# Kernel optimization log

Measured on AMD Instinct MI355X. Metric: run time of the kernel, lower is better.

The kernel has to match this reference:

```python
import jax, jax.numpy as jnp
import numpy as np

N_NODES = 50000
N_EDGES = 800000
IN_FEATURES = 256
HIDDEN = 128


def setup_inputs() -> dict:
    key = jax.random.key(0)
    k_x, k_r, k_c, k_v, k_w, k_b = jax.random.split(key, 6)
    x = jax.random.normal(k_x, (N_NODES, IN_FEATURES), dtype=jnp.float32)
    adj_row = jax.random.randint(k_r, (N_EDGES,), 0, N_NODES, dtype=jnp.int32)
    adj_col = jax.random.randint(k_c, (N_EDGES,), 0, N_NODES, dtype=jnp.int32)
    adj_val = jax.random.uniform(k_v, (N_EDGES,), dtype=jnp.float32)
    # Linear params: weight [hidden, in_features] (xavier-normal-ish), bias [hidden]
    std = float(np.sqrt(2.0 / (IN_FEATURES + HIDDEN)))
    W = jax.random.normal(k_w, (HIDDEN, IN_FEATURES), dtype=jnp.float32) * std
    b = jax.random.normal(k_b, (HIDDEN,), dtype=jnp.float32) * 0.01
    return {"x": x, "adj_row": adj_row, "adj_col": adj_col, "adj_val": adj_val, "W": W, "b": b}


def reference(x, adj_row, adj_col, adj_val, W, b):
    # support = Linear(x): [N, hidden]
    support = jnp.einsum('nf,hf->nh', x, W) + b
    # sparse adj @ support via edge-list gather + segment-sum scatter
    gathered = support[adj_col] * adj_val[:, None]          # [E, hidden]
    out = jax.ops.segment_sum(gathered, adj_row, num_segments=N_NODES)  # [N, hidden]
    return out
```

## Files before the change

kernel.cpp:

```cpp
#include <hip/hip_runtime.h>

#define N_NODES 50000
#define N_EDGES 800000
#define IN_F    256
#define HIDDEN  128

#define BUCKET_SZ 128
#define NB        391
#define NBS       512
#define EBLOCK    2048
#define EBLOCKS   391
#define LBLOCKS   782
#define CAP       2500
#define OV_CAP    4096

typedef __attribute__((ext_vector_type(8))) short bf16x8;
typedef __attribute__((ext_vector_type(4))) float f32x4;

__device__ inline unsigned short f2bf(float f) {
    unsigned u = __float_as_uint(f);
    u += 0x7FFF + ((u >> 16) & 1);
    return (unsigned short)(u >> 16);
}
__device__ inline bf16x8 cvt8(float4 a, float4 b) {
    bf16x8 r;
    r[0] = (short)f2bf(a.x); r[1] = (short)f2bf(a.y);
    r[2] = (short)f2bf(a.z); r[3] = (short)f2bf(a.w);
    r[4] = (short)f2bf(b.x); r[5] = (short)f2bf(b.y);
    r[6] = (short)f2bf(b.z); r[7] = (short)f2bf(b.w);
    return r;
}
__device__ inline float bfLo(unsigned u) { return __uint_as_float(u << 16); }
__device__ inline float bfHi(unsigned u) { return __uint_as_float(u & 0xFFFF0000u); }

__global__ __launch_bounds__(256) void fused_linear_partition_kernel(
    const float* __restrict__ x, const float* __restrict__ W,
    const float* __restrict__ bias, unsigned short* __restrict__ support,
    const int* __restrict__ adj_row, const int* __restrict__ adj_col,
    const float* __restrict__ adj_val, int* __restrict__ cursor,
    int2* __restrict__ part, int4* __restrict__ ovbuf, int* __restrict__ ovcnt)
{
    __shared__ __align__(16) char smem[32768];
    const int tid = threadIdx.x;

    if (blockIdx.x < EBLOCKS) {
        int2* lbuf  = (int2*)smem;
        int*  lofs  = (int*)(smem + 16384);
        int*  lcur  = (int*)(smem + 18432);
        int*  gbase = (int*)(smem + 20480);
        int*  tsum  = (int*)(smem + 22528);

        const int base = blockIdx.x * EBLOCK;
        const int n    = min(EBLOCK, N_EDGES - base);

        for (int i = tid; i < NBS; i += 256) lofs[i] = 0;
        __syncthreads();

        unsigned pk[8]; float pv[8];
#pragma unroll
        for (int i = 0; i < 8; ++i) {
            int e = base + tid + i * 256;
            bool ok = e < N_EDGES;
            int ee = ok ? e : 0;
            int r = adj_row[ee], c = adj_col[ee];
            float v = adj_val[ee];
            if (ok) {
                unsigned bk = (unsigned)r >> 7;
                pk[i] = (bk << 23) | (((unsigned)r & 127u) << 16) | (unsigned)c;
                pv[i] = v;
                atomicAdd(&lofs[bk], 1);
            } else pk[i] = 0xFFFFFFFFu;
        }
        __syncthreads();

        int s0 = lofs[tid * 2], s1 = lofs[tid * 2 + 1];
        int mysum = s0 + s1;
        tsum[tid] = mysum;
        __syncthreads();
#pragma unroll
        for (int off = 1; off < 256; off <<= 1) {
            int t = (tid >= off) ? tsum[tid - off] : 0;
            __syncthreads();
            tsum[tid] += t;
            __syncthreads();
        }
        int ex = tsum[tid] - mysum;
        lofs[tid * 2]     = ex;
        lofs[tid * 2 + 1] = ex + s0;
        __syncthreads();

        for (int b = tid; b < NB; b += 256) {
            int nb2 = (b * 2 + 2 < NBS) ? lofs[b + 1] : n;
            int c = lofs[b + 1] - lofs[b];
            (void)nb2;
            gbase[b] = (c > 0) ? atomicAdd(&cursor[b], c) : 0;
            lcur[b]  = lofs[b];
        }
        __syncthreads();

#pragma unroll
        for (int i = 0; i < 8; ++i) {
            if (pk[i] != 0xFFFFFFFFu) {
                unsigned bk = pk[i] >> 23;
                int p = atomicAdd(&lcur[bk], 1);
                lbuf[p] = make_int2((int)pk[i], __float_as_int(pv[i]));
            }
        }
        __syncthreads();

        for (int j = tid; j < n; j += 256) {
            int2 cv = lbuf[j];
            unsigned bk = ((unsigned)cv.x) >> 23;
            int loc = gbase[bk] + (j - lofs[bk]);
            if (loc < CAP) {
                part[(size_t)bk * CAP + loc] = make_int2(cv.x & 0x7FFFFF, cv.y);
            } else {
                int op = atomicAdd(ovcnt, 1);
                if (op < OV_CAP) {
                    int r = (int)(bk * BUCKET_SZ) + ((cv.x >> 16) & 127);
                    ovbuf[op] = make_int4(r, cv.x & 0xFFFF, cv.y, 0);
                }
            }
        }
    } else {
        short* wfrag = (short*)smem;

        const int bid  = blockIdx.x - EBLOCKS;
        const int lane = tid & 63;
        const int wave = tid >> 6;
        const int quad = lane >> 4;
        const int l16  = lane & 15;

        int m = bid * 64 + wave * 16 + l16;
        if (m >= N_NODES) m = N_NODES - 1;
        const float* xrow = x + (size_t)m * IN_F;

        f32x4 acc[8];
#pragma unroll
        for (int s = 0; s < 8; ++s) acc[s] = (f32x4){0.f, 0.f, 0.f, 0.f};

#pragma unroll
        for (int half = 0; half < 2; ++half) {
#pragma unroll
            for (int it = 0; it < 8; ++it) {
                const int f   = it * 256 + tid;
                const int ln  = f & 63;
                const int s   = (f >> 6) & 7;
                const int kc  = f >> 9;
                const int row = s * 16 + (ln & 15);
                const int k0  = (half * 4 + kc) * 32 + (ln >> 4) * 8;
                const float* wp = W + (size_t)row * IN_F + k0;
                float4 b0 = *(const float4*)wp;
                float4 b1 = *(const float4*)(wp + 4);
                *(bf16x8*)(&wfrag[(size_t)f * 8]) = cvt8(b0, b1);
            }
            __syncthreads();

#pragma unroll
            for (int kc = 0; kc < 4; ++kc) {
                const int k0 = (half * 4 + kc) * 32 + quad * 8;
                float4 a0 = *(const float4*)(xrow + k0);
                float4 a1 = *(const float4*)(xrow + k0 + 4);
                bf16x8 af = cvt8(a0, a1);
                const short* bbase = &wfrag[((size_t)(kc * 8) * 64 + lane) * 8];
#pragma unroll
                for (int s = 0; s < 8; ++s) {
                    bf16x8 bf = *(const bf16x8*)(bbase + (size_t)s * 64 * 8);
                    acc[s] = __builtin_amdgcn_mfma_f32_16x16x32_bf16(af, bf, acc[s], 0, 0, 0);
                }
            }
            __syncthreads();
        }

        const int rowBase = bid * 64 + wave * 16 + quad * 4;
#pragma unroll
        for (int reg = 0; reg < 4; ++reg) {
            const int r = rowBase + reg;
            if (r < N_NODES) {
#pragma unroll
                for (int s = 0; s < 8; ++s) {
                    const int col = s * 16 + l16;
                    float v = acc[s][reg] + bias[col];
                    support[(size_t)r * HIDDEN + col] = f2bf(v);
                }
            }
        }
    }
}

__global__ __launch_bounds__(512) void bucket_gather_kernel(
    const int* __restrict__ cursor, const int2* __restrict__ part,
    const unsigned int* __restrict__ support_u32, float* __restrict__ out)
{
    __shared__ int2 sbuf[CAP];
    __shared__ int  hist[BUCKET_SZ];
    __shared__ int  rp[BUCKET_SZ + 1];
    __shared__ int  cur[BUCKET_SZ];

    const int tid  = threadIdx.x;
    const int b    = blockIdx.x;
    const int n    = min(cursor[b], CAP);
    const int wave = tid >> 6;
    const int lane = tid & 63;

    if (tid < BUCKET_SZ) hist[tid] = 0;
    __syncthreads();

    int2 held[(CAP + 511) / 512];
    int  nheld = 0;
    const int2* pb = part + (size_t)b * CAP;
    for (int j = tid; j < n; j += 512) {
        int2 cv = pb[j];
        held[nheld++] = cv;
        atomicAdd(&hist[(cv.x >> 16) & 127], 1);
    }
    __syncthreads();

    if (tid < 64) {
        int a = hist[tid], c = hist[tid + 64];
        int ia = a, ic = c;
#pragma unroll
        for (int off = 1; off < 64; off <<= 1) {
            int ta = __shfl_up(ia, off);
            int tc = __shfl_up(ic, off);
            if (tid >= off) { ia += ta; ic += tc; }
        }
        int totA = __shfl(ia, 63);
        rp[tid + 1]      = ia;
        rp[tid + 65]     = totA + ic;
        if (tid == 0) rp[0] = 0;
        cur[tid]      = ia - a;
        cur[tid + 64] = totA + ic - c;
    }
    __syncthreads();

    for (int i = 0; i < nheld; ++i) {
        int r = (held[i].x >> 16) & 127;
        int p = atomicAdd(&cur[r], 1);
        sbuf[p] = held[i];
    }
    __syncthreads();

    const int rowLo = wave * 16;
#pragma unroll 1
    for (int r = rowLo; r < rowLo + 16; ++r) {
        const int grow = b * BUCKET_SZ + r;
        if (grow >= N_NODES) break;
        const int s = rp[r], e = rp[r + 1];
        float ax = 0.f, ay = 0.f;
        int j = s;
        for (; j + 3 < e; j += 4) {
            int2 c0 = sbuf[j],     c1 = sbuf[j + 1];
            int2 c2 = sbuf[j + 2], c3 = sbuf[j + 3];
            unsigned u0 = support_u32[(size_t)(c0.x & 0xFFFF) * 64 + lane];
            unsigned u1 = support_u32[(size_t)(c1.x & 0xFFFF) * 64 + lane];
            unsigned u2 = support_u32[(size_t)(c2.x & 0xFFFF) * 64 + lane];
            unsigned u3 = support_u32[(size_t)(c3.x & 0xFFFF) * 64 + lane];
            float v0 = __int_as_float(c0.y), v1 = __int_as_float(c1.y);
            float v2 = __int_as_float(c2.y), v3 = __int_as_float(c3.y);
            ax += v0 * bfLo(u0); ay += v0 * bfHi(u0);
            ax += v1 * bfLo(u1); ay += v1 * bfHi(u1);
            ax += v2 * bfLo(u2); ay += v2 * bfHi(u2);
            ax += v3 * bfLo(u3); ay += v3 * bfHi(u3);
        }
        for (; j < e; ++j) {
            int2 cv = sbuf[j];
            unsigned u = support_u32[(size_t)(cv.x & 0xFFFF) * 64 + lane];
            float v = __int_as_float(cv.y);
            ax += v * bfLo(u); ay += v * bfHi(u);
        }
        *(float2*)(out + (size_t)grow * HIDDEN + lane * 2) = make_float2(ax, ay);
    }
}

__global__ __launch_bounds__(256) void overflow_fix_kernel(
    const int* __restrict__ ovcnt, const int4* __restrict__ ovbuf,
    const unsigned int* __restrict__ support_u32, float* __restrict__ out)
{
    const int n    = min(*ovcnt, OV_CAP);
    const int wave = threadIdx.x >> 6;
    const int lane = threadIdx.x & 63;
    for (int j = wave; j < n; j += 4) {
        int4 o = ovbuf[j];
        unsigned u = support_u32[(size_t)o.y * 64 + lane];
        float v = __int_as_float(o.z);
        unsafeAtomicAdd(out + (size_t)o.x * HIDDEN + lane * 2,     v * bfLo(u));
        unsafeAtomicAdd(out + (size_t)o.x * HIDDEN + lane * 2 + 1, v * bfHi(u));
    }
}

extern "C" void kernel_launch(void* const* d_in, const int* in_sizes, int n_in,
                              void* d_out, int out_size, void* d_ws, size_t ws_size,
                              hipStream_t stream) {
    const float* x       = (const float*)d_in[0];
    const int*   adj_row = (const int*)d_in[1];
    const int*   adj_col = (const int*)d_in[2];
    const float* adj_val = (const float*)d_in[3];
    const float* W       = (const float*)d_in[4];
    const float* b       = (const float*)d_in[5];
    float* out = (float*)d_out;

    char* wsb = (char*)d_ws;
    const size_t off_support = 0;
    const size_t off_part    = off_support + (size_t)N_NODES * HIDDEN * 2;
    const size_t off_cursor  = off_part + (size_t)NB * CAP * 8;
    const size_t off_ovcnt   = off_cursor + (size_t)NB * 4;
    const size_t off_ovbuf   = (off_ovcnt + 4 + 15) & ~(size_t)15;

    unsigned short* support = (unsigned short*)(wsb + off_support);
    int2* part   = (int2*)(wsb + off_part);
    int*  cursor = (int*)(wsb + off_cursor);
    int*  ovcnt  = (int*)(wsb + off_ovcnt);
    int4* ovbuf  = (int4*)(wsb + off_ovbuf);

    hipMemsetAsync(cursor, 0, (size_t)(NB + 1) * 4, stream);

    fused_linear_partition_kernel<<<EBLOCKS + LBLOCKS, 256, 0, stream>>>(
        x, W, b, support, adj_row, adj_col, adj_val, cursor, part, ovbuf, ovcnt);
    bucket_gather_kernel<<<NB, 512, 0, stream>>>(
        cursor, part, (const unsigned int*)support, out);
    overflow_fix_kernel<<<1, 256, 0, stream>>>(
        ovcnt, ovbuf, (const unsigned int*)support, out);
}
```

Before: 188.9 us.

## Halve bucket size to 64 rows and fold overflow handling into gather

Rows are now partitioned into 782 buckets of 64 rows instead of 391 of 128, with the bucket id packed into the top 10 bits. The partition scan widens to 1024 bins, with four bins per thread. The gather kernel gets twice as many blocks, so more CUs are kept busy on the latency-bound support gathers. It now reads its partition twice instead of holding entries in registers, and scans the overflow buffer inline per row. That replaces the separate atomic overflow kernel and saves one launch. The cost is a per-row linear scan if overflow ever becomes non-empty, and slightly more workspace.

```diff
diff --git a/kernel.cpp b/kernel.cpp
--- a/kernel.cpp
+++ b/kernel.cpp
@@ -5,13 +5,13 @@
 #define IN_F    256
 #define HIDDEN  128
 
-#define BUCKET_SZ 128
-#define NB        391
-#define NBS       512
+#define BUCKET_SZ 64
+#define NB        782
+#define NBINS     1024
 #define EBLOCK    2048
 #define EBLOCKS   391
 #define LBLOCKS   782
-#define CAP       2500
+#define CAP       1300
 #define OV_CAP    4096
 
 typedef __attribute__((ext_vector_type(8))) short bf16x8;
@@ -46,14 +46,14 @@
     if (blockIdx.x < EBLOCKS) {
         int2* lbuf  = (int2*)smem;
         int*  lofs  = (int*)(smem + 16384);
-        int*  lcur  = (int*)(smem + 18432);
-        int*  gbase = (int*)(smem + 20480);
-        int*  tsum  = (int*)(smem + 22528);
+        int*  lcur  = (int*)(smem + 20480);
+        int*  gbase = (int*)(smem + 24576);
+        int*  tsum  = (int*)(smem + 27776);
 
         const int base = blockIdx.x * EBLOCK;
         const int n    = min(EBLOCK, N_EDGES - base);
 
-        for (int i = tid; i < NBS; i += 256) lofs[i] = 0;
+        for (int i = tid; i < NBINS; i += 256) lofs[i] = 0;
         __syncthreads();
 
         unsigned pk[8]; float pv[8];
@@ -65,16 +65,17 @@
             int r = adj_row[ee], c = adj_col[ee];
             float v = adj_val[ee];
             if (ok) {
-                unsigned bk = (unsigned)r >> 7;
-                pk[i] = (bk << 23) | (((unsigned)r & 127u) << 16) | (unsigned)c;
+                unsigned bk = (unsigned)r >> 6;
+                pk[i] = (bk << 22) | (((unsigned)r & 63u) << 16) | (unsigned)c;
                 pv[i] = v;
                 atomicAdd(&lofs[bk], 1);
             } else pk[i] = 0xFFFFFFFFu;
         }
         __syncthreads();
 
-        int s0 = lofs[tid * 2], s1 = lofs[tid * 2 + 1];
-        int mysum = s0 + s1;
+        int s0 = lofs[tid * 4], s1 = lofs[tid * 4 + 1];
+        int s2 = lofs[tid * 4 + 2], s3 = lofs[tid * 4 + 3];
+        int mysum = s0 + s1 + s2 + s3;
         tsum[tid] = mysum;
         __syncthreads();
 #pragma unroll
@@ -85,14 +86,14 @@
             __syncthreads();
         }
         int ex = tsum[tid] - mysum;
-        lofs[tid * 2]     = ex;
-        lofs[tid * 2 + 1] = ex + s0;
+        lofs[tid * 4]     = ex;
+        lofs[tid * 4 + 1] = ex + s0;
+        lofs[tid * 4 + 2] = ex + s0 + s1;
+        lofs[tid * 4 + 3] = ex + s0 + s1 + s2;
         __syncthreads();
 
         for (int b = tid; b < NB; b += 256) {
-            int nb2 = (b * 2 + 2 < NBS) ? lofs[b + 1] : n;
             int c = lofs[b + 1] - lofs[b];
-            (void)nb2;
             gbase[b] = (c > 0) ? atomicAdd(&cursor[b], c) : 0;
             lcur[b]  = lofs[b];
         }
@@ -101,7 +102,7 @@
 #pragma unroll
         for (int i = 0; i < 8; ++i) {
             if (pk[i] != 0xFFFFFFFFu) {
-                unsigned bk = pk[i] >> 23;
+                unsigned bk = pk[i] >> 22;
                 int p = atomicAdd(&lcur[bk], 1);
                 lbuf[p] = make_int2((int)pk[i], __float_as_int(pv[i]));
             }
@@ -110,14 +111,14 @@
 
         for (int j = tid; j < n; j += 256) {
             int2 cv = lbuf[j];
-            unsigned bk = ((unsigned)cv.x) >> 23;
+            unsigned bk = ((unsigned)cv.x) >> 22;
             int loc = gbase[bk] + (j - lofs[bk]);
             if (loc < CAP) {
-                part[(size_t)bk * CAP + loc] = make_int2(cv.x & 0x7FFFFF, cv.y);
+                part[(size_t)bk * CAP + loc] = make_int2(cv.x & 0x3FFFFF, cv.y);
             } else {
                 int op = atomicAdd(ovcnt, 1);
                 if (op < OV_CAP) {
-                    int r = (int)(bk * BUCKET_SZ) + ((cv.x >> 16) & 127);
+                    int r = (int)(bk * BUCKET_SZ) + ((cv.x >> 16) & 63);
                     ovbuf[op] = make_int4(r, cv.x & 0xFFFF, cv.y, 0);
                 }
             }
@@ -190,7 +191,9 @@
 
 __global__ __launch_bounds__(512) void bucket_gather_kernel(
     const int* __restrict__ cursor, const int2* __restrict__ part,
-    const unsigned int* __restrict__ support_u32, float* __restrict__ out)
+    const unsigned int* __restrict__ support_u32,
+    const int4* __restrict__ ovbuf, const int* __restrict__ ovcnt,
+    float* __restrict__ out)
 {
     __shared__ int2 sbuf[CAP];
     __shared__ int  hist[BUCKET_SZ];
@@ -202,48 +205,41 @@
     const int n    = min(cursor[b], CAP);
     const int wave = tid >> 6;
     const int lane = tid & 63;
+    const int n_ov = min(*ovcnt, OV_CAP);
 
     if (tid < BUCKET_SZ) hist[tid] = 0;
     __syncthreads();
 
-    int2 held[(CAP + 511) / 512];
-    int  nheld = 0;
     const int2* pb = part + (size_t)b * CAP;
     for (int j = tid; j < n; j += 512) {
+        atomicAdd(&hist[(pb[j].x >> 16) & 63], 1);
+    }
+    __syncthreads();
+
+    if (tid < 64) {
+        int a = hist[tid];
+        int ia = a;
+#pragma unroll
+        for (int off = 1; off < 64; off <<= 1) {
+            int t = __shfl_up(ia, off);
+            if (tid >= off) ia += t;
+        }
+        rp[tid + 1] = ia;
+        if (tid == 0) rp[0] = 0;
+        cur[tid] = ia - a;
+    }
+    __syncthreads();
+
+    for (int j = tid; j < n; j += 512) {
         int2 cv = pb[j];
-        held[nheld++] = cv;
-        atomicAdd(&hist[(cv.x >> 16) & 127], 1);
+        int p = atomicAdd(&cur[(cv.x >> 16) & 63], 1);
+        sbuf[p] = cv;
     }
     __syncthreads();
 
-    if (tid < 64) {
-        int a = hist[tid], c = hist[tid + 64];
-        int ia = a, ic = c;
-#pragma unroll
-        for (int off = 1; off < 64; off <<= 1) {
-            int ta = __shfl_up(ia, off);
-            int tc = __shfl_up(ic, off);
-            if (tid >= off) { ia += ta; ic += tc; }
-        }
-        int totA = __shfl(ia, 63);
-        rp[tid + 1]      = ia;
-        rp[tid + 65]     = totA + ic;
-        if (tid == 0) rp[0] = 0;
-        cur[tid]      = ia - a;
-        cur[tid + 64] = totA + ic - c;
-    }
-    __syncthreads();
-
-    for (int i = 0; i < nheld; ++i) {
-        int r = (held[i].x >> 16) & 127;
-        int p = atomicAdd(&cur[r], 1);
-        sbuf[p] = held[i];
-    }
-    __syncthreads();
-
-    const int rowLo = wave * 16;
+    const int rowLo = wave * 8;
 #pragma unroll 1
-    for (int r = rowLo; r < rowLo + 16; ++r) {
+    for (int r = rowLo; r < rowLo + 8; ++r) {
         const int grow = b * BUCKET_SZ + r;
         if (grow >= N_NODES) break;
         const int s = rp[r], e = rp[r + 1];
@@ -269,23 +265,15 @@
             float v = __int_as_float(cv.y);
             ax += v * bfLo(u); ay += v * bfHi(u);
         }
+        for (int t = 0; t < n_ov; ++t) {
+            int4 o = ovbuf[t];
+            if (o.x == grow) {
+                unsigned u = support_u32[(size_t)o.y * 64 + lane];
+                float v = __int_as_float(o.z);
+                ax += v * bfLo(u); ay += v * bfHi(u);
+            }
+        }
         *(float2*)(out + (size_t)grow * HIDDEN + lane * 2) = make_float2(ax, ay);
-    }
-}
-
-__global__ __launch_bounds__(256) void overflow_fix_kernel(
-    const int* __restrict__ ovcnt, const int4* __restrict__ ovbuf,
-    const unsigned int* __restrict__ support_u32, float* __restrict__ out)
-{
-    const int n    = min(*ovcnt, OV_CAP);
-    const int wave = threadIdx.x >> 6;
-    const int lane = threadIdx.x & 63;
-    for (int j = wave; j < n; j += 4) {
-        int4 o = ovbuf[j];
-        unsigned u = support_u32[(size_t)o.y * 64 + lane];
-        float v = __int_as_float(o.z);
-        unsafeAtomicAdd(out + (size_t)o.x * HIDDEN + lane * 2,     v * bfLo(u));
-        unsafeAtomicAdd(out + (size_t)o.x * HIDDEN + lane * 2 + 1, v * bfHi(u));
     }
 }
 
@@ -318,7 +306,5 @@
     fused_linear_partition_kernel<<<EBLOCKS + LBLOCKS, 256, 0, stream>>>(
         x, W, b, support, adj_row, adj_col, adj_val, cursor, part, ovbuf, ovcnt);
     bucket_gather_kernel<<<NB, 512, 0, stream>>>(
-        cursor, part, (const unsigned int*)support, out);
-    overflow_fix_kernel<<<1, 256, 0, stream>>>(
-        ovcnt, ovbuf, (const unsigned int*)support, out);
-}
+        cursor, part, (const unsigned int*)support, ovbuf, ovcnt, out);
+}
```

Measured after the change: 163.2 us. 1.16x faster.
